# Kernel optimization log

Hardware: AMD Instinct MI355X
Metric: run time of the kernel (lower is better)

## Reference

```python
import jax, jax.numpy as jnp
import numpy as np

B, L, ENC_IN, C_OUT = 4, 2048, 64, 64
D_MODEL, N_HEADS, D_FF, E_LAYERS = 1024, 16, 4096, 4
CA_K = 5  # ChannelAttention1D kernel: int(|log2(1024)+1|/2)=5 (odd)


def _layer_norm(x, w, b, eps=1e-5):
    m = x.mean(-1, keepdims=True)
    v = ((x - m) ** 2).mean(-1, keepdims=True)
    return (x - m) * jax.lax.rsqrt(v + eps) * w + b


def _flow_attention(q, k, v):
    # q,k,v: [B, L, H, D] -> work in [B, H, L, D]
    q = jax.nn.sigmoid(jnp.swapaxes(q, 1, 2))
    k = jax.nn.sigmoid(jnp.swapaxes(k, 1, 2))
    v = jnp.swapaxes(v, 1, 2)
    eps = 1e-6
    Lq = q.shape[2]
    S = k.shape[2]
    nr = 1.0 / jnp.einsum('bhld,bhd->bhl', q + eps, k.sum(axis=2) + eps)
    nc = 1.0 / jnp.einsum('bhsd,bhd->bhs', k + eps, q.sum(axis=2) + eps)
    nrr = jnp.einsum('bhld,bhd->bhl', q + eps, (k * nc[..., None]).sum(axis=2) + eps)
    ncr = jnp.einsum('bhsd,bhd->bhs', k + eps, (q * nr[..., None]).sum(axis=2) + eps)
    nrr = jax.nn.sigmoid(nrr * (float(Lq) / float(S)))
    ncr = jax.nn.softmax(ncr, axis=-1) * S
    kv = jnp.einsum('bhsd,bhse->bhde', k, v * ncr[..., None])  # [B,H,D,Dv]
    out = jnp.einsum('bhld,bhde->bhle', q, kv) * nr[..., None] * nrr[..., None]
    return jnp.swapaxes(out, 1, 2)  # [B, L, H, Dv]


def _token_embed(x, w):
    # x: [B, L, Cin]; circular conv1d kernel=3, pad=1, no bias
    xt = jnp.swapaxes(x, 1, 2)  # [B, Cin, L]
    xt = jnp.concatenate([xt[..., -1:], xt, xt[..., :1]], axis=-1)
    y = jax.lax.conv_general_dilated(xt, w, (1,), 'VALID',
                                     dimension_numbers=('NCH', 'OIH', 'NCH'))
    return jnp.swapaxes(y, 1, 2)  # [B, L, d_model]


def _channel_att(x, w):
    # x: [B, L, C]; squeeze over L, conv over channel axis, sigmoid gate
    y = x.mean(axis=1, keepdims=True)  # [B, 1, C]
    pad = CA_K // 2
    yp = jnp.pad(y, ((0, 0), (0, 0), (pad, pad)))
    yc = jax.lax.conv_general_dilated(yp, w.reshape(1, 1, CA_K), (1,), 'VALID',
                                      dimension_numbers=('NCH', 'OIH', 'NCH'))
    return x * jax.nn.sigmoid(yc)


def _encoder_layer(x, Wq, bq, Wk, bk, Wv, bv, Wo, bo,
                   ln1w, ln1b, ln2w, ln2b, c1w, c1b, c2w, c2b):
    Bx, Lx, _ = x.shape
    q = (x @ Wq.T + bq).reshape(Bx, Lx, N_HEADS, -1)
    k = (x @ Wk.T + bk).reshape(Bx, Lx, N_HEADS, -1)
    v = (x @ Wv.T + bv).reshape(Bx, Lx, N_HEADS, -1)
    a = _flow_attention(q, k, v).reshape(Bx, Lx, -1)
    a = a @ Wo.T + bo
    x = _layer_norm(x + a, ln1w, ln1b)
    y = jax.nn.relu(jnp.einsum('bld,fd->blf', x, c1w) + c1b)  # conv1 k=1
    y = jnp.einsum('blf,df->bld', y, c2w) + c2b               # conv2 k=1
    return _layer_norm(x + y, ln2w, ln2b)


def setup_inputs() -> dict:
    key = jax.random.key(0)
    ks = jax.random.split(key, 16)
    s = 0.02
    E, D, F = E_LAYERS, D_MODEL, D_FF
    inp = {
        'x': jax.random.normal(ks[0], (B, L, ENC_IN), jnp.float32),
        'tok_conv_w': jax.random.normal(ks[1], (D, ENC_IN, 3), jnp.float32) * s,
        'Wq': jax.random.normal(ks[2], (E, D, D), jnp.float32) * s,
        'bq': jnp.zeros((E, D), jnp.float32),
        'Wk': jax.random.normal(ks[3], (E, D, D), jnp.float32) * s,
        'bk': jnp.zeros((E, D), jnp.float32),
        'Wv': jax.random.normal(ks[4], (E, D, D), jnp.float32) * s,
        'bv': jnp.zeros((E, D), jnp.float32),
        'Wo': jax.random.normal(ks[5], (E, D, D), jnp.float32) * s,
        'bo': jnp.zeros((E, D), jnp.float32),
        'conv1_w': jax.random.normal(ks[6], (E, F, D), jnp.float32) * s,
        'conv1_b': jnp.zeros((E, F), jnp.float32),
        'conv2_w': jax.random.normal(ks[7], (E, D, F), jnp.float32) * s,
        'conv2_b': jnp.zeros((E, D), jnp.float32),
        'ln1_w': jnp.ones((E, D), jnp.float32),
        'ln1_b': jnp.zeros((E, D), jnp.float32),
        'ln2_w': jnp.ones((E, D), jnp.float32),
        'ln2_b': jnp.zeros((E, D), jnp.float32),
        'ca_w': jax.random.normal(ks[8], (E, CA_K), jnp.float32) * 0.2,
        'lnf_w': jnp.ones((D,), jnp.float32),
        'lnf_b': jnp.zeros((D,), jnp.float32),
        'proj_w': jax.random.normal(ks[9], (C_OUT, D), jnp.float32) * s,
        'proj_b': jnp.zeros((C_OUT,), jnp.float32),
    }
    return inp


def reference(x, tok_conv_w, Wq, bq, Wk, bk, Wv, bv, Wo, bo,
              conv1_w, conv1_b, conv2_w, conv2_b,
              ln1_w, ln1_b, ln2_w, ln2_b, ca_w,
              lnf_w, lnf_b, proj_w, proj_b):
    h = _token_embed(x, tok_conv_w)  # dropout = identity (eval)
    for i in range(E_LAYERS):
        h = _encoder_layer(h, Wq[i], bq[i], Wk[i], bk[i], Wv[i], bv[i], Wo[i], bo[i],
                           ln1_w[i], ln1_b[i], ln2_w[i], ln2_b[i],
                           conv1_w[i], conv1_b[i], conv2_w[i], conv2_b[i])
        h = _channel_att(h, ca_w[i])
    # Encoder re-applies the last attention layer after the conv loop (faithful)
    i = E_LAYERS - 1
    h = _encoder_layer(h, Wq[i], bq[i], Wk[i], bk[i], Wv[i], bv[i], Wo[i], bo[i],
                       ln1_w[i], ln1_b[i], ln2_w[i], ln2_b[i],
                       conv1_w[i], conv1_b[i], conv2_w[i], conv2_b[i])
    h = _layer_norm(h, lnf_w, lnf_b)
    return h @ proj_w.T + proj_b
```

## Files before the change

kernel.cpp:

```cpp
#include <hip/hip_runtime.h>
#include <stdint.h>

#define L_SEQ 2048
#define DM 1024
#define NH 16
#define DFF 4096
#define NB 4
#define ROWS (NB * L_SEQ)

typedef __attribute__((ext_vector_type(8))) __bf16 bf16x8;
typedef __attribute__((ext_vector_type(4))) float f32x4;

__device__ __forceinline__ float bf2f(unsigned short u) {
  union { unsigned int i; float f; } x; x.i = ((unsigned int)u) << 16; return x.f;
}
__device__ __forceinline__ unsigned short f2bf(float f) {
  union { float f; unsigned int i; } x; x.f = f;
  unsigned int r = x.i + 0x7FFFu + ((x.i >> 16) & 1u);
  return (unsigned short)(r >> 16);
}

typedef __attribute__((address_space(3))) void lds_void;
typedef const __attribute__((address_space(1))) void gbl_void;

__device__ __forceinline__ void stage16(const void* g, void* ldsbase) {
  __builtin_amdgcn_global_load_lds((gbl_void*)g, (lds_void*)ldsbase, 16, 0, 0);
}

__global__ __launch_bounds__(256)
void gemm_bt(const unsigned short* __restrict__ A,
             const unsigned short* __restrict__ B,
             const float* __restrict__ bias,
             unsigned short* __restrict__ C16,
             float* __restrict__ C32,
             int K, int lda, int ldc, int n_limit, int act)
{
  __shared__ __attribute__((aligned(16))) unsigned short As[128 * 32];
  __shared__ __attribute__((aligned(16))) unsigned short Bs[128 * 32];
  const int tid  = threadIdx.x;
  const int wave = tid >> 6, lane = tid & 63;
  const int wm = (wave & 1) << 6, wn = (wave >> 1) << 6;
  const int l16 = lane & 15, quad = lane >> 4;

  const unsigned short* Ab = A + (size_t)blockIdx.x * 128 * lda;
  const unsigned short* Bb = B + (size_t)blockIdx.y * 128 * K;

  const int srow = (wave << 4) + (lane >> 2);
  const int scol = (lane & 3) << 3;

  f32x4 acc[4][4] = {};

  for (int k0 = 0; k0 < K; k0 += 32) {
    const size_t aoff = (size_t)srow * lda + k0 + scol;
    const size_t boff = (size_t)srow * K   + k0 + scol;
    stage16(Ab + aoff,                    &As[(wave * 16) * 32]);
    stage16(Ab + aoff + (size_t)64 * lda, &As[(wave * 16 + 64) * 32]);
    stage16(Bb + boff,                    &Bs[(wave * 16) * 32]);
    stage16(Bb + boff + (size_t)64 * K,   &Bs[(wave * 16 + 64) * 32]);
    __syncthreads();

    bf16x8 af[4], bfr[4];
#pragma unroll
    for (int mi = 0; mi < 4; mi++)
      af[mi] = *(const bf16x8*)&As[(wm + mi * 16 + l16) * 32 + quad * 8];
#pragma unroll
    for (int ni = 0; ni < 4; ni++)
      bfr[ni] = *(const bf16x8*)&Bs[(wn + ni * 16 + l16) * 32 + quad * 8];
#pragma unroll
    for (int mi = 0; mi < 4; mi++)
#pragma unroll
      for (int ni = 0; ni < 4; ni++)
        acc[mi][ni] = __builtin_amdgcn_mfma_f32_16x16x32_bf16(af[mi], bfr[ni], acc[mi][ni], 0, 0, 0);
    __syncthreads();
  }

  const int row0 = (int)blockIdx.x * 128 + wm + quad * 4;
  const int col0 = (int)blockIdx.y * 128 + wn + l16;
#pragma unroll
  for (int ni = 0; ni < 4; ni++) {
    const int col = col0 + ni * 16;
    if (col >= n_limit) continue;
    const float bv = bias ? bias[col] : 0.0f;
    const bool sig = (act == 2) || (act == 3 && col < 2048);
#pragma unroll
    for (int mi = 0; mi < 4; mi++) {
#pragma unroll
      for (int r = 0; r < 4; r++) {
        const int row = row0 + mi * 16 + r;
        float v = acc[mi][ni][r] + bv;
        if (act == 1) v = fmaxf(v, 0.0f);
        else if (sig) v = 1.0f / (1.0f + __expf(-v));
        if (C32) C32[(size_t)row * ldc + col] = v;
        if (C16) C16[(size_t)row * ldc + col] = f2bf(v);
      }
    }
  }
}

#define AFRAG(bb, mi, ks) (*(const bf16x8*)(smb + (bb) + ((mi) << 11) + ((ks) << 10) + lb))
#define BFRAG(bb, nj, ks) (*(const bf16x8*)(smb + (bb) + 32768 + ((nj) << 11) + ((ks) << 10) + lb))

#define LOAD_A(bb, qm) \
  fa[0][0] = AFRAG(bb, wm8 + (qm)*4 + 0, 0); fa[0][1] = AFRAG(bb, wm8 + (qm)*4 + 0, 1); \
  fa[1][0] = AFRAG(bb, wm8 + (qm)*4 + 1, 0); fa[1][1] = AFRAG(bb, wm8 + (qm)*4 + 1, 1); \
  fa[2][0] = AFRAG(bb, wm8 + (qm)*4 + 2, 0); fa[2][1] = AFRAG(bb, wm8 + (qm)*4 + 2, 1); \
  fa[3][0] = AFRAG(bb, wm8 + (qm)*4 + 3, 0); fa[3][1] = AFRAG(bb, wm8 + (qm)*4 + 3, 1);

#define LOAD_B(bb, qn) \
  fb[(qn)*2+0][0] = BFRAG(bb, wn4 + (qn)*2 + 0, 0); fb[(qn)*2+0][1] = BFRAG(bb, wn4 + (qn)*2 + 0, 1); \
  fb[(qn)*2+1][0] = BFRAG(bb, wn4 + (qn)*2 + 1, 0); fb[(qn)*2+1][1] = BFRAG(bb, wn4 + (qn)*2 + 1, 1);

#define MM(mi, nj) \
  acc[mi][nj] = __builtin_amdgcn_mfma_f32_16x16x32_bf16(fa[(mi)&3][0], fb[nj][0], acc[mi][nj], 0, 0, 0); \
  acc[mi][nj] = __builtin_amdgcn_mfma_f32_16x16x32_bf16(fa[(mi)&3][1], fb[nj][1], acc[mi][nj], 0, 0, 0);

#define MFMA_QUAD(qm, qn) \
  MM((qm)*4+0, (qn)*2+0) MM((qm)*4+0, (qn)*2+1) \
  MM((qm)*4+1, (qn)*2+0) MM((qm)*4+1, (qn)*2+1) \
  MM((qm)*4+2, (qn)*2+0) MM((qm)*4+2, (qn)*2+1) \
  MM((qm)*4+3, (qn)*2+0) MM((qm)*4+3, (qn)*2+1)

#define PH_MFMA(qm, qn) \
  __builtin_amdgcn_s_barrier(); \
  asm volatile("s_waitcnt lgkmcnt(0)" ::: "memory"); \
  __builtin_amdgcn_sched_barrier(0); \
  __builtin_amdgcn_s_setprio(1); \
  MFMA_QUAD(qm, qn); \
  __builtin_amdgcn_s_setprio(0); \
  __builtin_amdgcn_sched_barrier(0); \
  __builtin_amdgcn_s_barrier();

__global__ __launch_bounds__(512, 2)
void gemm256(const unsigned short* __restrict__ A,
             const unsigned short* __restrict__ B,
             const float* __restrict__ bias,
             unsigned short* __restrict__ C16,
             float* __restrict__ C32,
             int K, int lda, int ldc, int n_limit, int act, int nb)
{
  __shared__ __attribute__((aligned(16))) unsigned short sm[65536];
  char* smb = (char*)sm;

  const int tid  = threadIdx.x;
  const int wave = tid >> 6, lane = tid & 63;
  const int l16 = lane & 15, quad = lane >> 4;
  const int lb = lane << 4;
  const int wm = wave >> 2, wn = wave & 3;
  const int wm8 = wm * 8, wn4 = wn * 4;

  const int nwg  = (int)gridDim.x;
  const int orig = (int)blockIdx.x;
  const int qq = nwg >> 3, rr = nwg & 7;
  const int xcd = orig & 7, loc = orig >> 3;
  const int wgid = (xcd < rr ? xcd * (qq + 1) : rr * (qq + 1) + (xcd - rr) * qq) + loc;
  const int bx = wgid / nb, by = wgid % nb;

  const unsigned short* Ab = A + (size_t)bx * 256 * lda;
  const unsigned short* Bb = B + (size_t)by * 256 * K;

  const int rb0 = ((wave >> 1) << 4) + l16;
  const int cb0 = ((wave & 1) << 5) + (quad << 3);

  const int T = K >> 6;

  auto stageHalf = [&](int bufbyte, int h, int t) {
    const unsigned short* src;
    size_t ld;
    if (h < 2) { ld = (size_t)lda; src = Ab + (size_t)((h & 1) * 128 + rb0) * ld + (size_t)t * 64 + cb0; }
    else       { ld = (size_t)K;   src = Bb + (size_t)((h & 1) * 128 + rb0) * ld + (size_t)t * 64 + cb0; }
    char* dst = smb + bufbyte + h * 16384 + wave * 1024;
    stage16(src, dst);
    stage16(src + 64 * ld, dst + 8192);
  };

  bf16x8 fa[4][2], fb[4][2];
  f32x4 acc[8][4] = {};

  stageHalf(0, 0, 0); stageHalf(0, 1, 0); stageHalf(0, 2, 0); stageHalf(0, 3, 0);
  if (T > 1) {
    stageHalf(1 << 16, 0, 1);
    asm volatile("s_waitcnt vmcnt(2)" ::: "memory");
  } else {
    asm volatile("s_waitcnt vmcnt(0)" ::: "memory");
  }
  __builtin_amdgcn_sched_barrier(0);
  __builtin_amdgcn_s_barrier();

  for (int t = 0; t < T; ++t) {
    const int bb  = (t & 1) << 16;
    const int nbb = bb ^ (1 << 16);
    const bool st1 = (t + 1 < T), st2 = (t + 2 < T);

    LOAD_A(bb, 0)
    LOAD_B(bb, 0)
    if (st1) stageHalf(nbb, 1, t + 1);
    PH_MFMA(0, 0)

    LOAD_B(bb, 1)
    if (st1) stageHalf(nbb, 2, t + 1);
    PH_MFMA(0, 1)

    LOAD_A(bb, 1)
    if (st1) stageHalf(nbb, 3, t + 1);
    PH_MFMA(1, 1)

    if (st2) {
      stageHalf(bb, 0, t + 2);
      asm volatile("s_waitcnt vmcnt(2)" ::: "memory");
    } else {
      asm volatile("s_waitcnt vmcnt(0)" ::: "memory");
    }
    __builtin_amdgcn_sched_barrier(0);
    __builtin_amdgcn_s_barrier();
    __builtin_amdgcn_s_setprio(1);
    MFMA_QUAD(1, 0)
    __builtin_amdgcn_s_setprio(0);
    __builtin_amdgcn_sched_barrier(0);
    __builtin_amdgcn_s_barrier();
  }

  const int row0 = bx * 256 + wm * 128 + quad * 4;
  const int col0 = by * 256 + wn * 64 + l16;
#pragma unroll
  for (int nj = 0; nj < 4; ++nj) {
    const int col = col0 + nj * 16;
    if (col >= n_limit) continue;
    const float bv = bias ? bias[col] : 0.0f;
    const bool sig = (act == 2) || (act == 3 && col < 2048);
#pragma unroll
    for (int mi = 0; mi < 8; ++mi) {
#pragma unroll
      for (int r = 0; r < 4; ++r) {
        const int row = row0 + mi * 16 + r;
        float v = acc[mi][nj][r] + bv;
        if (act == 1) v = fmaxf(v, 0.0f);
        else if (sig) v = 1.0f / (1.0f + __expf(-v));
        if (C32) C32[(size_t)row * ldc + col] = v;
        if (C16) C16[(size_t)row * ldc + col] = f2bf(v);
      }
    }
  }
}


__global__ __launch_bounds__(256)
void fa_sums(const unsigned short* __restrict__ Q, const unsigned short* __restrict__ K,
             int ld, float* __restrict__ ksp, float* __restrict__ qsp)
{
  const int bh = blockIdx.x, chunk = blockIdx.y;
  const size_t base = ((size_t)(bh >> 4) * L_SEQ) * ld + (size_t)(bh & 15) * 64;
  const int t = threadIdx.x, lane = t & 63, wave = t >> 6;
  __shared__ float red[256];
  float ks = 0.f, qs = 0.f;
  const int l0 = chunk * 256 + wave * 64;
  for (int i = 0; i < 64; i++) {
    const size_t idx = base + (size_t)(l0 + i) * ld + lane;
    ks += bf2f(K[idx]);
    qs += bf2f(Q[idx]);
  }
  red[t] = ks; __syncthreads();
  if (t < 64) ksp[(bh * 8 + chunk) * 64 + t] = red[t] + red[t + 64] + red[t + 128] + red[t + 192];
  __syncthreads();
  red[t] = qs; __syncthreads();
  if (t < 64) qsp[(bh * 8 + chunk) * 64 + t] = red[t] + red[t + 64] + red[t + 128] + red[t + 192];
}

__global__ __launch_bounds__(256)
void fa_rows1(const unsigned short* __restrict__ Q, const unsigned short* __restrict__ K,
              int ld, const float* __restrict__ ksp, const float* __restrict__ qsp,
              float* __restrict__ nr, float* __restrict__ t1p, float* __restrict__ t2p)
{
  const int bh = blockIdx.x, chunk = blockIdx.y;
  const size_t base = ((size_t)(bh >> 4) * L_SEQ) * ld + (size_t)(bh & 15) * 64;
  const int t = threadIdx.x, lane = t & 63, wave = t >> 6;
  const float eps = 1e-6f;
  __shared__ float s_kse[64], s_qse[64], red[256];
  if (t < 64) {
    float s = 0.f;
    for (int j = 0; j < 8; j++) s += ksp[(bh * 8 + j) * 64 + t];
    s_kse[t] = s + eps;
  } else if (t < 128) {
    const int d = t - 64;
    float s = 0.f;
    for (int j = 0; j < 8; j++) s += qsp[(bh * 8 + j) * 64 + d];
    s_qse[d] = s + eps;
  }
  __syncthreads();
  const float kse = s_kse[lane], qse = s_qse[lane];
  float t1a = 0.f, t2a = 0.f;
  for (int i = 0; i < 32; i++) {
    const int l = chunk * 128 + wave + 4 * i;
    const size_t idx = base + (size_t)l * ld + lane;
    const float q = bf2f(Q[idx]), k = bf2f(K[idx]);
    float a = (q + eps) * kse;
    float c = (k + eps) * qse;
#pragma unroll
    for (int off = 32; off; off >>= 1) { a += __shfl_xor(a, off); c += __shfl_xor(c, off); }
    const float nrl = 1.f / a, ncl = 1.f / c;
    if (lane == 0) nr[bh * L_SEQ + l] = nrl;
    t1a += k * ncl;
    t2a += q * nrl;
  }
  red[t] = t1a; __syncthreads();
  if (t < 64) t1p[(bh * 16 + chunk) * 64 + t] = red[t] + red[t + 64] + red[t + 128] + red[t + 192];
  __syncthreads();
  red[t] = t2a; __syncthreads();
  if (t < 64) t2p[(bh * 16 + chunk) * 64 + t] = red[t] + red[t + 64] + red[t + 128] + red[t + 192];
}

__global__ __launch_bounds__(256)
void fa_rows2(const unsigned short* __restrict__ Q, const unsigned short* __restrict__ K,
              int ld, const float* __restrict__ t1p, const float* __restrict__ t2p,
              float* __restrict__ nr, float* __restrict__ sc)
{
  const int bh = blockIdx.x, chunk = blockIdx.y;
  const size_t base = ((size_t)(bh >> 4) * L_SEQ) * ld + (size_t)(bh & 15) * 64;
  const int t = threadIdx.x, lane = t & 63, wave = t >> 6;
  const float eps = 1e-6f;
  __shared__ float s_t1e[64], s_t2e[64];
  if (t < 64) {
    float s = 0.f;
    for (int j = 0; j < 16; j++) s += t1p[(bh * 16 + j) * 64 + t];
    s_t1e[t] = s + eps;
  } else if (t < 128) {
    const int d = t - 64;
    float s = 0.f;
    for (int j = 0; j < 16; j++) s += t2p[(bh * 16 + j) * 64 + d];
    s_t2e[d] = s + eps;
  }
  __syncthreads();
  const float t1e = s_t1e[lane], t2e = s_t2e[lane];
  for (int i = 0; i < 32; i++) {
    const int l = chunk * 128 + wave + 4 * i;
    const size_t idx = base + (size_t)l * ld + lane;
    const float q = bf2f(Q[idx]), k = bf2f(K[idx]);
    float a = (q + eps) * t1e;
    float c = (k + eps) * t2e;
#pragma unroll
    for (int off = 32; off; off >>= 1) { a += __shfl_xor(a, off); c += __shfl_xor(c, off); }
    if (lane == 0) {
      nr[bh * L_SEQ + l] *= 1.f / (1.f + __expf(-a));
      sc[bh * L_SEQ + l] = c;
    }
  }
}

__global__ __launch_bounds__(256)
void fa_softmax(float* __restrict__ sc, float* __restrict__ kv)
{
  const int bh = blockIdx.x, t = threadIdx.x;
  __shared__ float red[256];
  float4* kvz = (float4*)(kv + bh * 64 * 64);
  for (int j = 0; j < 4; j++) kvz[t + 256 * j] = make_float4(0.f, 0.f, 0.f, 0.f);

  float* row = sc + bh * L_SEQ;
  float m = -3.4e38f;
  for (int l = t; l < L_SEQ; l += 256) m = fmaxf(m, row[l]);
  red[t] = m; __syncthreads();
  for (int s = 128; s > 0; s >>= 1) { if (t < s) red[t] = fmaxf(red[t], red[t + s]); __syncthreads(); }
  const float mx = red[0];
  __syncthreads();
  float ps = 0.f;
  float pv[8];
#pragma unroll
  for (int j = 0; j < 8; j++) {
    const int l = t + 256 * j;
    pv[j] = __expf(row[l] - mx);
    ps += pv[j];
  }
  red[t] = ps; __syncthreads();
  for (int s = 128; s > 0; s >>= 1) { if (t < s) red[t] += red[t + s]; __syncthreads(); }
  const float scale = (float)L_SEQ / red[0];
#pragma unroll
  for (int j = 0; j < 8; j++) row[t + 256 * j] = pv[j] * scale;
}

__global__ __launch_bounds__(256)
void fa_kv(const unsigned short* __restrict__ K, const unsigned short* __restrict__ V,
           int ld, const float* __restrict__ sc, float* __restrict__ kv)
{
  const int bh = blockIdx.x, chunk = blockIdx.y;
  const size_t base = ((size_t)(bh >> 4) * L_SEQ) * ld + (size_t)(bh & 15) * 64;
  const int t = threadIdx.x, lane = t & 63, wave = t >> 6;
  const int l16 = lane & 15, quad = lane >> 4;
  __shared__ __attribute__((aligned(16))) unsigned short s_kT[64 * 72];
  __shared__ __attribute__((aligned(16))) unsigned short s_vT[64 * 72];

  f32x4 acc5[4] = {};
  for (int sub = 0; sub < 2; sub++) {
    const int l0 = chunk * 128 + sub * 64;
#pragma unroll
    for (int it = 0; it < 4; it++) {
      const int task = it * 256 + t;
      const int l = task >> 4;
      const int g = task & 15;
      const size_t gidx = base + (size_t)(l0 + l) * ld + g * 4;
      const ushort4 k4 = *(const ushort4*)(K + gidx);
      const ushort4 v4 = *(const ushort4*)(V + gidx);
      const float wgt = sc[bh * L_SEQ + l0 + l];
      s_kT[(g * 4 + 0) * 72 + l] = k4.x;
      s_kT[(g * 4 + 1) * 72 + l] = k4.y;
      s_kT[(g * 4 + 2) * 72 + l] = k4.z;
      s_kT[(g * 4 + 3) * 72 + l] = k4.w;
      s_vT[(g * 4 + 0) * 72 + l] = f2bf(bf2f(v4.x) * wgt);
      s_vT[(g * 4 + 1) * 72 + l] = f2bf(bf2f(v4.y) * wgt);
      s_vT[(g * 4 + 2) * 72 + l] = f2bf(bf2f(v4.z) * wgt);
      s_vT[(g * 4 + 3) * 72 + l] = f2bf(bf2f(v4.w) * wgt);
    }
    __syncthreads();
#pragma unroll
    for (int ks = 0; ks < 2; ks++) {
      const bf16x8 af = *(const bf16x8*)&s_kT[(wave * 16 + l16) * 72 + ks * 32 + quad * 8];
#pragma unroll
      for (int et = 0; et < 4; et++) {
        const bf16x8 bf = *(const bf16x8*)&s_vT[(et * 16 + l16) * 72 + ks * 32 + quad * 8];
        acc5[et] = __builtin_amdgcn_mfma_f32_16x16x32_bf16(af, bf, acc5[et], 0, 0, 0);
      }
    }
    __syncthreads();
  }
#pragma unroll
  for (int et = 0; et < 4; et++)
#pragma unroll
    for (int r = 0; r < 4; r++)
      atomicAdd(&kv[bh * 4096 + (wave * 16 + quad * 4 + r) * 64 + et * 16 + l16], acc5[et][r]);
}

__global__ __launch_bounds__(256)
void fa_out(const unsigned short* __restrict__ Q, int ld, const float* __restrict__ kv,
            const float* __restrict__ nr, unsigned short* O)
{
  const int bh = blockIdx.x, chunk = blockIdx.y;
  const size_t base = ((size_t)(bh >> 4) * L_SEQ) * ld + (size_t)(bh & 15) * 64;
  const int t = threadIdx.x, lane = t & 63, wave = t >> 6;
  const int l16 = lane & 15, quad = lane >> 4;
  __shared__ __attribute__((aligned(16))) unsigned short s_kvT[64 * 72];

#pragma unroll
  for (int j = 0; j < 16; j++) {
    const int i = t + 256 * j;
    const int d = i >> 6, e = i & 63;
    s_kvT[e * 72 + d] = f2bf(kv[bh * 4096 + i]);
  }
  __syncthreads();

  bf16x8 bfr6[4][2];
#pragma unroll
  for (int et = 0; et < 4; et++)
#pragma unroll
    for (int ks = 0; ks < 2; ks++)
      bfr6[et][ks] = *(const bf16x8*)&s_kvT[(et * 16 + l16) * 72 + ks * 32 + quad * 8];

#pragma unroll
  for (int ti = 0; ti < 2; ti++) {
    const int l0 = chunk * 128 + (wave * 2 + ti) * 16;
    f32x4 oc[4] = {};
#pragma unroll
    for (int ks = 0; ks < 2; ks++) {
      const bf16x8 aq = *(const bf16x8*)(Q + base + (size_t)(l0 + l16) * ld + ks * 32 + quad * 8);
#pragma unroll
      for (int et = 0; et < 4; et++)
        oc[et] = __builtin_amdgcn_mfma_f32_16x16x32_bf16(aq, bfr6[et][ks], oc[et], 0, 0, 0);
    }
#pragma unroll
    for (int r = 0; r < 4; r++) {
      const int l = l0 + quad * 4 + r;
      const float scl = nr[bh * L_SEQ + l];
#pragma unroll
      for (int et = 0; et < 4; et++)
        O[base + (size_t)l * ld + et * 16 + l16] = f2bf(oc[et][r] * scl);
    }
  }
}

__global__ __launch_bounds__(256)
void ln_fused(const float* res, const float* __restrict__ add,
              const float* __restrict__ w, const float* __restrict__ bb,
              float* out32, unsigned short* out16)
{
  const int row = blockIdx.x * 4 + (threadIdx.x >> 6);
  const int lane = threadIdx.x & 63;
  const size_t roff = (size_t)row * DM;
  const float4* rp = (const float4*)(res + roff);
  const float4* ap = add ? (const float4*)(add + roff) : nullptr;

  float x[16], s = 0.f, s2 = 0.f;
#pragma unroll
  for (int q4 = 0; q4 < 4; q4++) {
    float4 v = rp[lane * 4 + q4];
    if (ap) { float4 a = ap[lane * 4 + q4]; v.x += a.x; v.y += a.y; v.z += a.z; v.w += a.w; }
    x[q4 * 4 + 0] = v.x; x[q4 * 4 + 1] = v.y; x[q4 * 4 + 2] = v.z; x[q4 * 4 + 3] = v.w;
    s += v.x + v.y + v.z + v.w;
    s2 += v.x * v.x + v.y * v.y + v.z * v.z + v.w * v.w;
  }
#pragma unroll
  for (int off = 32; off; off >>= 1) { s += __shfl_xor(s, off); s2 += __shfl_xor(s2, off); }
  const float mean = s * (1.f / DM);
  const float var = s2 * (1.f / DM) - mean * mean;
  const float rstd = rsqrtf(var + 1e-5f);
#pragma unroll
  for (int j = 0; j < 16; j++) {
    const int c = lane * 16 + j;
    x[j] = (x[j] - mean) * rstd * w[c] + bb[c];
  }
  if (out32) {
    float4* op = (float4*)(out32 + roff);
#pragma unroll
    for (int q4 = 0; q4 < 4; q4++) {
      float4 v; v.x = x[q4*4+0]; v.y = x[q4*4+1]; v.z = x[q4*4+2]; v.w = x[q4*4+3];
      op[lane * 4 + q4] = v;
    }
  }
  if (out16) {
#pragma unroll
    for (int q4 = 0; q4 < 4; q4++) {
      ushort4 u;
      u.x = f2bf(x[q4*4+0]); u.y = f2bf(x[q4*4+1]); u.z = f2bf(x[q4*4+2]); u.w = f2bf(x[q4*4+3]);
      *(ushort4*)(out16 + roff + lane * 16 + q4 * 4) = u;
    }
  }
}

__global__ void ca_zero(float* __restrict__ ybar) {
  const int i = blockIdx.x * 256 + threadIdx.x;
  if (i < NB * DM) ybar[i] = 0.f;
}
__global__ void ca_mean(const unsigned short* __restrict__ H16, float* __restrict__ ybar) {
  const int b = blockIdx.x, cc = blockIdx.y, lc = blockIdx.z;
  const int c = cc * 256 + threadIdx.x;
  float s = 0.f;
  for (int l = lc * 256; l < lc * 256 + 256; l++)
    s += bf2f(H16[((size_t)(b * L_SEQ + l)) * DM + c]);
  atomicAdd(&ybar[b * DM + c], s);
}
__global__ void ca_gate(const float* __restrict__ ybar, const float* __restrict__ cw,
                        float* __restrict__ gate) {
  const int i = blockIdx.x * 256 + threadIdx.x;
  if (i >= NB * DM) return;
  const int b = i >> 10, c = i & 1023;
  float acc = 0.f;
#pragma unroll
  for (int j = 0; j < 5; j++) {
    const int cc = c + j - 2;
    const float yv = (cc >= 0 && cc < DM) ? ybar[b * DM + cc] * (1.f / L_SEQ) : 0.f;
    acc += cw[j] * yv;
  }
  gate[i] = 1.f / (1.f + __expf(-acc));
}
__global__ void ca_apply(float* __restrict__ H32, unsigned short* __restrict__ H16,
                         const float* __restrict__ gate) {
  const size_t i = ((size_t)blockIdx.x * 256 + threadIdx.x) * 4;
  const int row = (int)(i >> 10);
  const int b = row >> 11;
  const int c = (int)(i & 1023);
  float4 v = *(float4*)(H32 + i);
  v.x *= gate[b * DM + c + 0];
  v.y *= gate[b * DM + c + 1];
  v.z *= gate[b * DM + c + 2];
  v.w *= gate[b * DM + c + 3];
  *(float4*)(H32 + i) = v;
  unsigned short* hp = H16 + i;
  hp[0] = f2bf(v.x); hp[1] = f2bf(v.y); hp[2] = f2bf(v.z); hp[3] = f2bf(v.w);
}

__global__ void embed_gather(const float* __restrict__ x, unsigned short* __restrict__ Ae) {
  const int i = blockIdx.x * 256 + threadIdx.x;
  if (i >= ROWS * 192) return;
  const int row = i / 192, kk = i % 192;
  const int t3 = kk >> 6, c = kk & 63;
  const int b = row >> 11, l = row & 2047;
  const int ls = (l + t3 - 1 + L_SEQ) & 2047;
  Ae[i] = f2bf(x[((size_t)(b * L_SEQ + ls)) * 64 + c]);
}
__global__ void embed_repack(const float* __restrict__ w, unsigned short* __restrict__ We) {
  const int i = blockIdx.x * 256 + threadIdx.x;
  if (i >= DM * 192) return;
  const int f = i / 192, kk = i % 192;
  const int t3 = kk >> 6, c = kk & 63;
  We[i] = f2bf(w[(f * 64 + c) * 3 + t3]);
}
__global__ void pad_proj(const float* __restrict__ pw, unsigned short* __restrict__ Wp) {
  const int i = blockIdx.x * 256 + threadIdx.x;
  if (i >= 128 * DM) return;
  Wp[i] = ((i >> 10) < 64) ? f2bf(pw[i]) : (unsigned short)0;
}
__global__ void pack_qkv_bias(const float* __restrict__ bq, const float* __restrict__ bk,
                              const float* __restrict__ bv, float* __restrict__ bqkv) {
  const int i = blockIdx.x * 256 + threadIdx.x;
  if (i >= 3072) return;
  bqkv[i] = (i < 1024) ? bq[i] : (i < 2048 ? bk[i - 1024] : bv[i - 2048]);
}
__global__ void cvt_layer_weights(const float* __restrict__ Wq, const float* __restrict__ Wk,
                                  const float* __restrict__ Wv, const float* __restrict__ Wo,
                                  const float* __restrict__ c1, const float* __restrict__ c2,
                                  unsigned short* __restrict__ Wl, unsigned short* __restrict__ WlFF) {
  const int g = blockIdx.x * 256 + threadIdx.x;
  const int i = g << 2;
  const float* src; unsigned short* dst;
  if (i < (1 << 22)) {
    const int w = i >> 20, off = i & ((1 << 20) - 1);
    const float* srcs[4] = {Wq, Wk, Wv, Wo};
    src = srcs[w] + off; dst = Wl + (w << 20) + off;
  } else {
    const int j = i - (1 << 22);
    const int w = j >> 22, off = j & ((1 << 22) - 1);
    src = (w ? c2 : c1) + off; dst = WlFF + (w << 22) + off;
  }
  const float4 v = *(const float4*)src;
  ushort4 u; u.x = f2bf(v.x); u.y = f2bf(v.y); u.z = f2bf(v.z); u.w = f2bf(v.w);
  *(ushort4*)dst = u;
}

extern "C" void kernel_launch(void* const* d_in, const int* in_sizes, int n_in,
                              void* d_out, int out_size, void* d_ws, size_t ws_size,
                              hipStream_t stream) {
  const float* x     = (const float*)d_in[0];
  const float* tokw  = (const float*)d_in[1];
  const float* Wq    = (const float*)d_in[2];
  const float* bq    = (const float*)d_in[3];
  const float* Wk    = (const float*)d_in[4];
  const float* bk    = (const float*)d_in[5];
  const float* Wv    = (const float*)d_in[6];
  const float* bv    = (const float*)d_in[7];
  const float* Wo    = (const float*)d_in[8];
  const float* bo    = (const float*)d_in[9];
  const float* c1w   = (const float*)d_in[10];
  const float* c1b   = (const float*)d_in[11];
  const float* c2w   = (const float*)d_in[12];
  const float* c2b   = (const float*)d_in[13];
  const float* ln1w  = (const float*)d_in[14];
  const float* ln1b  = (const float*)d_in[15];
  const float* ln2w  = (const float*)d_in[16];
  const float* ln2b  = (const float*)d_in[17];
  const float* caw   = (const float*)d_in[18];
  const float* lnfw  = (const float*)d_in[19];
  const float* lnfb  = (const float*)d_in[20];
  const float* projw = (const float*)d_in[21];
  const float* projb = (const float*)d_in[22];

  char* ws = (char*)d_ws;
  float*          R32 = (float*)(ws);
  unsigned short* R16 = (unsigned short*)(ws + ((size_t)32 << 20));
  float*          A32 = (float*)(ws + ((size_t)48 << 20));
  unsigned short* U   = (unsigned short*)(ws + ((size_t)80 << 20));
  unsigned short* QKV16 = U;
  unsigned short* F16   = U;
  char* fa = ws + ((size_t)128 << 20);
  float* fa_nr  = (float*)(fa);
  float* fa_sc  = (float*)(fa + (512 << 10));
  float* fa_ksp = (float*)(fa + (1024 << 10));
  float* fa_qsp = (float*)(fa + (1152 << 10));
  float* fa_t1p = (float*)(fa + (1280 << 10));
  float* fa_t2p = (float*)(fa + (1792 << 10));
  float* fa_kvb = (float*)(fa + (2304 << 10));
  unsigned short* Wl   = (unsigned short*)(ws + ((size_t)144 << 20));
  unsigned short* WlFF = (unsigned short*)(ws + ((size_t)152 << 20));
  char* misc = ws + ((size_t)168 << 20);
  float*          ybar = (float*)misc;
  float*          gate = (float*)(misc + (16 << 10));
  float*          bqkv = (float*)(misc + (32 << 10));
  unsigned short* We   = (unsigned short*)(misc + (64 << 10));
  unsigned short* Wp   = (unsigned short*)(misc + (512 << 10));

  const int BIG = 1 << 30;
  auto gemm = [&](const unsigned short* A, const unsigned short* B, const float* bias,
                  unsigned short* C16, float* C32, int N, int K, int lda, int ldc,
                  int nlim, int act) {
    if ((N & 255) == 0 && (K & 63) == 0) {
      const int nb = N >> 8;
      const int nwg = (ROWS >> 8) * nb;
      gemm256<<<dim3(nwg), dim3(512), 0, stream>>>(A, B, bias, C16, C32, K, lda, ldc, nlim, act, nb);
    } else {
      dim3 grid(ROWS / 128, N / 128);
      gemm_bt<<<grid, dim3(256), 0, stream>>>(A, B, bias, C16, C32, K, lda, ldc, nlim, act);
    }
  };

  embed_gather<<<(ROWS * 192 + 255) / 256, 256, 0, stream>>>(x, U);
  embed_repack<<<(DM * 192 + 255) / 256, 256, 0, stream>>>(tokw, We);
  gemm(U, We, nullptr, R16, R32, DM, 192, 192, DM, BIG, 0);

  for (int it = 0; it < 5; it++) {
    const int i = (it < 4) ? it : 3;
    if (it != 4) {
      cvt_layer_weights<<<(3 << 20) / 256, 256, 0, stream>>>(
          Wq + ((size_t)i << 20), Wk + ((size_t)i << 20),
          Wv + ((size_t)i << 20), Wo + ((size_t)i << 20),
          c1w + ((size_t)i << 22), c2w + ((size_t)i << 22), Wl, WlFF);
      pack_qkv_bias<<<12, 256, 0, stream>>>(bq + i * DM, bk + i * DM, bv + i * DM, bqkv);
    }
    const unsigned short* Wo16 = Wl + (3 << 20);
    const unsigned short* C116 = WlFF;
    const unsigned short* C216 = WlFF + (1 << 22);

    gemm(R16, Wl, bqkv, QKV16, nullptr, 3072, DM, DM, 3072, BIG, 3);

    const unsigned short* Qp = QKV16;
    const unsigned short* Kp = QKV16 + 1024;
    unsigned short*       Vp = QKV16 + 2048;

    fa_sums   <<<dim3(64, 8),  256, 0, stream>>>(Qp, Kp, 3072, fa_ksp, fa_qsp);
    fa_rows1  <<<dim3(64, 16), 256, 0, stream>>>(Qp, Kp, 3072, fa_ksp, fa_qsp, fa_nr, fa_t1p, fa_t2p);
    fa_rows2  <<<dim3(64, 16), 256, 0, stream>>>(Qp, Kp, 3072, fa_t1p, fa_t2p, fa_nr, fa_sc);
    fa_softmax<<<dim3(64),     256, 0, stream>>>(fa_sc, fa_kvb);
    fa_kv     <<<dim3(64, 16), 256, 0, stream>>>(Kp, Vp, 3072, fa_sc, fa_kvb);
    fa_out    <<<dim3(64, 16), 256, 0, stream>>>(Qp, 3072, fa_kvb, fa_nr, Vp);

    gemm(Vp, Wo16, bo + i * DM, nullptr, A32, DM, DM, 3072, DM, BIG, 0);
    ln_fused<<<ROWS / 4, 256, 0, stream>>>(R32, A32, ln1w + i * DM, ln1b + i * DM, R32, R16);
    gemm(R16, C116, c1b + i * DFF, F16, nullptr, DFF, DM, DM, DFF, BIG, 1);
    gemm(F16, C216, c2b + i * DM, nullptr, A32, DM, DFF, DFF, DM, BIG, 0);
    ln_fused<<<ROWS / 4, 256, 0, stream>>>(R32, A32, ln2w + i * DM, ln2b + i * DM, R32, R16);

    if (it < 4) {
      ca_zero<<<16, 256, 0, stream>>>(ybar);
      ca_mean<<<dim3(NB, 4, 8), 256, 0, stream>>>(R16, ybar);
      ca_gate<<<16, 256, 0, stream>>>(ybar, caw + i * 5, gate);
      ca_apply<<<(ROWS * DM / 4) / 256, 256, 0, stream>>>(R32, R16, gate);
    }
  }

  ln_fused<<<ROWS / 4, 256, 0, stream>>>(R32, nullptr, lnfw, lnfb, nullptr, U);
  pad_proj<<<(128 * DM + 255) / 256, 256, 0, stream>>>(projw, Wp);
  gemm(U, Wp, projb, nullptr, (float*)d_out, 128, DM, DM, 64, 64, 0);

  (void)in_sizes; (void)n_in; (void)out_size; (void)ws_size;
}
```

Measured before the change: 3.159 ms.

## Add pipelined 128x128 GEMM for small-N shapes and deepen gemm256 prefetch

Replaces the simple gemm_bt kernel with a new gemm128 kernel. gemm128 uses 64-wide K tiles, double-buffered global_load_lds staging, an XCD-aware workgroup remap and phased MFMA blocks with barriers. The dispatcher now sends N<3072 GEMMs (e.g. N=1024 projections, embed, N=64 proj) to gemm128 instead of gemm256, which gives more workgroups for better CU occupancy. gemm256 now stages the whole next tile upfront and prefetches two tiles ahead with vmcnt(8). Risks: the N=64 output projection and the K=192 embed shapes rely on gemm128 handling the n_limit and K bounds correctly.

```diff
diff --git a/kernel.cpp b/kernel.cpp
--- a/kernel.cpp
+++ b/kernel.cpp
@@ -27,75 +27,7 @@
   __builtin_amdgcn_global_load_lds((gbl_void*)g, (lds_void*)ldsbase, 16, 0, 0);
 }
 
-__global__ __launch_bounds__(256)
-void gemm_bt(const unsigned short* __restrict__ A,
-             const unsigned short* __restrict__ B,
-             const float* __restrict__ bias,
-             unsigned short* __restrict__ C16,
-             float* __restrict__ C32,
-             int K, int lda, int ldc, int n_limit, int act)
-{
-  __shared__ __attribute__((aligned(16))) unsigned short As[128 * 32];
-  __shared__ __attribute__((aligned(16))) unsigned short Bs[128 * 32];
-  const int tid  = threadIdx.x;
-  const int wave = tid >> 6, lane = tid & 63;
-  const int wm = (wave & 1) << 6, wn = (wave >> 1) << 6;
-  const int l16 = lane & 15, quad = lane >> 4;
-
-  const unsigned short* Ab = A + (size_t)blockIdx.x * 128 * lda;
-  const unsigned short* Bb = B + (size_t)blockIdx.y * 128 * K;
-
-  const int srow = (wave << 4) + (lane >> 2);
-  const int scol = (lane & 3) << 3;
-
-  f32x4 acc[4][4] = {};
-
-  for (int k0 = 0; k0 < K; k0 += 32) {
-    const size_t aoff = (size_t)srow * lda + k0 + scol;
-    const size_t boff = (size_t)srow * K   + k0 + scol;
-    stage16(Ab + aoff,                    &As[(wave * 16) * 32]);
-    stage16(Ab + aoff + (size_t)64 * lda, &As[(wave * 16 + 64) * 32]);
-    stage16(Bb + boff,                    &Bs[(wave * 16) * 32]);
-    stage16(Bb + boff + (size_t)64 * K,   &Bs[(wave * 16 + 64) * 32]);
-    __syncthreads();
-
-    bf16x8 af[4], bfr[4];
-#pragma unroll
-    for (int mi = 0; mi < 4; mi++)
-      af[mi] = *(const bf16x8*)&As[(wm + mi * 16 + l16) * 32 + quad * 8];
-#pragma unroll
-    for (int ni = 0; ni < 4; ni++)
-      bfr[ni] = *(const bf16x8*)&Bs[(wn + ni * 16 + l16) * 32 + quad * 8];
-#pragma unroll
-    for (int mi = 0; mi < 4; mi++)
-#pragma unroll
-      for (int ni = 0; ni < 4; ni++)
-        acc[mi][ni] = __builtin_amdgcn_mfma_f32_16x16x32_bf16(af[mi], bfr[ni], acc[mi][ni], 0, 0, 0);
-    __syncthreads();
-  }
-
-  const int row0 = (int)blockIdx.x * 128 + wm + quad * 4;
-  const int col0 = (int)blockIdx.y * 128 + wn + l16;
-#pragma unroll
-  for (int ni = 0; ni < 4; ni++) {
-    const int col = col0 + ni * 16;
-    if (col >= n_limit) continue;
-    const float bv = bias ? bias[col] : 0.0f;
-    const bool sig = (act == 2) || (act == 3 && col < 2048);
-#pragma unroll
-    for (int mi = 0; mi < 4; mi++) {
-#pragma unroll
-      for (int r = 0; r < 4; r++) {
-        const int row = row0 + mi * 16 + r;
-        float v = acc[mi][ni][r] + bv;
-        if (act == 1) v = fmaxf(v, 0.0f);
-        else if (sig) v = 1.0f / (1.0f + __expf(-v));
-        if (C32) C32[(size_t)row * ldc + col] = v;
-        if (C16) C16[(size_t)row * ldc + col] = f2bf(v);
-      }
-    }
-  }
-}
+#define MFMA1(d, a, b) (d) = __builtin_amdgcn_mfma_f32_16x16x32_bf16((a), (b), (d), 0, 0, 0)
 
 #define AFRAG(bb, mi, ks) (*(const bf16x8*)(smb + (bb) + ((mi) << 11) + ((ks) << 10) + lb))
 #define BFRAG(bb, nj, ks) (*(const bf16x8*)(smb + (bb) + 32768 + ((nj) << 11) + ((ks) << 10) + lb))
@@ -120,12 +52,13 @@
   MM((qm)*4+2, (qn)*2+0) MM((qm)*4+2, (qn)*2+1) \
   MM((qm)*4+3, (qn)*2+0) MM((qm)*4+3, (qn)*2+1)
 
-#define PH_MFMA(qm, qn) \
+#define PH_OPEN \
   __builtin_amdgcn_s_barrier(); \
   asm volatile("s_waitcnt lgkmcnt(0)" ::: "memory"); \
   __builtin_amdgcn_sched_barrier(0); \
-  __builtin_amdgcn_s_setprio(1); \
-  MFMA_QUAD(qm, qn); \
+  __builtin_amdgcn_s_setprio(1);
+
+#define PH_CLOSE \
   __builtin_amdgcn_s_setprio(0); \
   __builtin_amdgcn_sched_barrier(0); \
   __builtin_amdgcn_s_barrier();
@@ -178,8 +111,9 @@
 
   stageHalf(0, 0, 0); stageHalf(0, 1, 0); stageHalf(0, 2, 0); stageHalf(0, 3, 0);
   if (T > 1) {
-    stageHalf(1 << 16, 0, 1);
-    asm volatile("s_waitcnt vmcnt(2)" ::: "memory");
+    stageHalf(1 << 16, 0, 1); stageHalf(1 << 16, 1, 1);
+    stageHalf(1 << 16, 2, 1); stageHalf(1 << 16, 3, 1);
+    asm volatile("s_waitcnt vmcnt(8)" ::: "memory");
   } else {
     asm volatile("s_waitcnt vmcnt(0)" ::: "memory");
   }
@@ -187,26 +121,29 @@
   __builtin_amdgcn_s_barrier();
 
   for (int t = 0; t < T; ++t) {
-    const int bb  = (t & 1) << 16;
-    const int nbb = bb ^ (1 << 16);
-    const bool st1 = (t + 1 < T), st2 = (t + 2 < T);
+    const int bb = (t & 1) << 16;
+    const bool st2 = (t + 2 < T);
 
     LOAD_A(bb, 0)
     LOAD_B(bb, 0)
-    if (st1) stageHalf(nbb, 1, t + 1);
-    PH_MFMA(0, 0)
+    PH_OPEN
+    MFMA_QUAD(0, 0)
+    PH_CLOSE
 
     LOAD_B(bb, 1)
-    if (st1) stageHalf(nbb, 2, t + 1);
-    PH_MFMA(0, 1)
+    PH_OPEN
+    MFMA_QUAD(0, 1)
+    PH_CLOSE
 
     LOAD_A(bb, 1)
-    if (st1) stageHalf(nbb, 3, t + 1);
-    PH_MFMA(1, 1)
+    if (st2) { stageHalf(bb, 2, t + 2); stageHalf(bb, 3, t + 2); }
+    PH_OPEN
+    MFMA_QUAD(1, 1)
+    PH_CLOSE
 
     if (st2) {
-      stageHalf(bb, 0, t + 2);
-      asm volatile("s_waitcnt vmcnt(2)" ::: "memory");
+      stageHalf(bb, 0, t + 2); stageHalf(bb, 1, t + 2);
+      asm volatile("s_waitcnt vmcnt(8)" ::: "memory");
     } else {
       asm volatile("s_waitcnt vmcnt(0)" ::: "memory");
     }
@@ -214,9 +151,7 @@
     __builtin_amdgcn_s_barrier();
     __builtin_amdgcn_s_setprio(1);
     MFMA_QUAD(1, 0)
-    __builtin_amdgcn_s_setprio(0);
-    __builtin_amdgcn_sched_barrier(0);
-    __builtin_amdgcn_s_barrier();
+    PH_CLOSE
   }
 
   const int row0 = bx * 256 + wm * 128 + quad * 4;
@@ -229,6 +164,152 @@
     const bool sig = (act == 2) || (act == 3 && col < 2048);
 #pragma unroll
     for (int mi = 0; mi < 8; ++mi) {
+#pragma unroll
+      for (int r = 0; r < 4; ++r) {
+        const int row = row0 + mi * 16 + r;
+        float v = acc[mi][nj][r] + bv;
+        if (act == 1) v = fmaxf(v, 0.0f);
+        else if (sig) v = 1.0f / (1.0f + __expf(-v));
+        if (C32) C32[(size_t)row * ldc + col] = v;
+        if (C16) C16[(size_t)row * ldc + col] = f2bf(v);
+      }
+    }
+  }
+}
+
+#define AFRAG1(bb, mig, ks) (*(const bf16x8*)(smb + (bb) + (((mig) * 2 + (ks)) << 10) + lb))
+#define BFRAG1(bb, njg, ks) (*(const bf16x8*)(smb + (bb) + 16384 + (((njg) * 2 + (ks)) << 10) + lb))
+
+#define PH128(...) \
+  __builtin_amdgcn_s_barrier(); \
+  asm volatile("s_waitcnt lgkmcnt(0)" ::: "memory"); \
+  __builtin_amdgcn_sched_barrier(0); \
+  __builtin_amdgcn_s_setprio(1); \
+  __VA_ARGS__ \
+  __builtin_amdgcn_s_setprio(0); \
+  __builtin_amdgcn_sched_barrier(0); \
+  __builtin_amdgcn_s_barrier();
+
+__global__ __launch_bounds__(256, 2)
+void gemm128(const unsigned short* __restrict__ A,
+             const unsigned short* __restrict__ B,
+             const float* __restrict__ bias,
+             unsigned short* __restrict__ C16,
+             float* __restrict__ C32,
+             int K, int lda, int ldc, int n_limit, int act, int nb)
+{
+  __shared__ __attribute__((aligned(16))) unsigned short sm[32768];
+  char* smb = (char*)sm;
+  const int tid  = threadIdx.x;
+  const int wave = tid >> 6, lane = tid & 63;
+  const int l16 = lane & 15, quad = lane >> 4;
+  const int lb = lane << 4;
+  const int wm = wave >> 1, wn = wave & 1;
+  const int wm4 = wm * 4, wn4 = wn * 4;
+
+  const int nwg  = (int)gridDim.x;
+  const int orig = (int)blockIdx.x;
+  const int qq = nwg >> 3, rr = nwg & 7;
+  const int xcd = orig & 7, loc = orig >> 3;
+  const int wgid = (xcd < rr ? xcd * (qq + 1) : rr * (qq + 1) + (xcd - rr) * qq) + loc;
+  const int bx = wgid / nb, by = wgid % nb;
+
+  const unsigned short* Ab = A + (size_t)bx * 128 * lda;
+  const unsigned short* Bb = B + (size_t)by * 128 * K;
+
+  const int rb0 = ((wave >> 1) << 4) + l16;
+  const int cb0 = ((wave & 1) << 5) + (quad << 3);
+
+  const int T = K >> 6;
+
+  auto stageA = [&](int bufbyte, int t) {
+    const unsigned short* s0 = Ab + (size_t)rb0 * lda + (size_t)t * 64 + cb0;
+    char* d = smb + bufbyte + wave * 1024;
+    stage16(s0, d);
+    stage16(s0 + (size_t)32 * lda, d + 4096);
+    stage16(s0 + (size_t)64 * lda, d + 8192);
+    stage16(s0 + (size_t)96 * lda, d + 12288);
+  };
+  auto stageB = [&](int bufbyte, int t) {
+    const unsigned short* s0 = Bb + (size_t)rb0 * K + (size_t)t * 64 + cb0;
+    char* d = smb + bufbyte + 16384 + wave * 1024;
+    stage16(s0, d);
+    stage16(s0 + (size_t)32 * K, d + 4096);
+    stage16(s0 + (size_t)64 * K, d + 8192);
+    stage16(s0 + (size_t)96 * K, d + 12288);
+  };
+
+  bf16x8 fa[2][2], fb01[2][2], fb23[2][2];
+  f32x4 acc[4][4] = {};
+
+  stageA(0, 0); stageB(0, 0);
+  if (T > 1) {
+    stageA(32768, 1); stageB(32768, 1);
+    asm volatile("s_waitcnt vmcnt(8)" ::: "memory");
+  } else {
+    asm volatile("s_waitcnt vmcnt(0)" ::: "memory");
+  }
+  __builtin_amdgcn_sched_barrier(0);
+  __builtin_amdgcn_s_barrier();
+
+  for (int t = 0; t < T; ++t) {
+    const int bb = (t & 1) << 15;
+    const bool st2 = (t + 2 < T);
+
+    fa[0][0] = AFRAG1(bb, wm4 + 0, 0); fa[0][1] = AFRAG1(bb, wm4 + 0, 1);
+    fa[1][0] = AFRAG1(bb, wm4 + 1, 0); fa[1][1] = AFRAG1(bb, wm4 + 1, 1);
+    fb01[0][0] = BFRAG1(bb, wn4 + 0, 0); fb01[0][1] = BFRAG1(bb, wn4 + 0, 1);
+    fb01[1][0] = BFRAG1(bb, wn4 + 1, 0); fb01[1][1] = BFRAG1(bb, wn4 + 1, 1);
+    PH128(
+      MFMA1(acc[0][0], fa[0][0], fb01[0][0]); MFMA1(acc[0][0], fa[0][1], fb01[0][1]);
+      MFMA1(acc[0][1], fa[0][0], fb01[1][0]); MFMA1(acc[0][1], fa[0][1], fb01[1][1]);
+      MFMA1(acc[1][0], fa[1][0], fb01[0][0]); MFMA1(acc[1][0], fa[1][1], fb01[0][1]);
+      MFMA1(acc[1][1], fa[1][0], fb01[1][0]); MFMA1(acc[1][1], fa[1][1], fb01[1][1]);
+    )
+
+    fb23[0][0] = BFRAG1(bb, wn4 + 2, 0); fb23[0][1] = BFRAG1(bb, wn4 + 2, 1);
+    fb23[1][0] = BFRAG1(bb, wn4 + 3, 0); fb23[1][1] = BFRAG1(bb, wn4 + 3, 1);
+    PH128(
+      MFMA1(acc[0][2], fa[0][0], fb23[0][0]); MFMA1(acc[0][2], fa[0][1], fb23[0][1]);
+      MFMA1(acc[0][3], fa[0][0], fb23[1][0]); MFMA1(acc[0][3], fa[0][1], fb23[1][1]);
+      MFMA1(acc[1][2], fa[1][0], fb23[0][0]); MFMA1(acc[1][2], fa[1][1], fb23[0][1]);
+      MFMA1(acc[1][3], fa[1][0], fb23[1][0]); MFMA1(acc[1][3], fa[1][1], fb23[1][1]);
+    )
+
+    fa[0][0] = AFRAG1(bb, wm4 + 2, 0); fa[0][1] = AFRAG1(bb, wm4 + 2, 1);
+    fa[1][0] = AFRAG1(bb, wm4 + 3, 0); fa[1][1] = AFRAG1(bb, wm4 + 3, 1);
+    if (st2) stageB(bb, t + 2);
+    PH128(
+      MFMA1(acc[2][2], fa[0][0], fb23[0][0]); MFMA1(acc[2][2], fa[0][1], fb23[0][1]);
+      MFMA1(acc[2][3], fa[0][0], fb23[1][0]); MFMA1(acc[2][3], fa[0][1], fb23[1][1]);
+      MFMA1(acc[3][2], fa[1][0], fb23[0][0]); MFMA1(acc[3][2], fa[1][1], fb23[0][1]);
+      MFMA1(acc[3][3], fa[1][0], fb23[1][0]); MFMA1(acc[3][3], fa[1][1], fb23[1][1]);
+    )
+
+    if (st2) {
+      stageA(bb, t + 2);
+      asm volatile("s_waitcnt vmcnt(8)" ::: "memory");
+    } else {
+      asm volatile("s_waitcnt vmcnt(0)" ::: "memory");
+    }
+    PH128(
+      MFMA1(acc[2][0], fa[0][0], fb01[0][0]); MFMA1(acc[2][0], fa[0][1], fb01[0][1]);
+      MFMA1(acc[2][1], fa[0][0], fb01[1][0]); MFMA1(acc[2][1], fa[0][1], fb01[1][1]);
+      MFMA1(acc[3][0], fa[1][0], fb01[0][0]); MFMA1(acc[3][0], fa[1][1], fb01[0][1]);
+      MFMA1(acc[3][1], fa[1][0], fb01[1][0]); MFMA1(acc[3][1], fa[1][1], fb01[1][1]);
+    )
+  }
+
+  const int row0 = bx * 128 + wm * 64 + quad * 4;
+  const int col0 = by * 128 + wn * 64 + l16;
+#pragma unroll
+  for (int nj = 0; nj < 4; ++nj) {
+    const int col = col0 + nj * 16;
+    if (col >= n_limit) continue;
+    const float bv = bias ? bias[col] : 0.0f;
+    const bool sig = (act == 2) || (act == 3 && col < 2048);
+#pragma unroll
+    for (int mi = 0; mi < 4; ++mi) {
 #pragma unroll
       for (int r = 0; r < 4; ++r) {
         const int row = row0 + mi * 16 + r;
@@ -666,13 +747,14 @@
   auto gemm = [&](const unsigned short* A, const unsigned short* B, const float* bias,
                   unsigned short* C16, float* C32, int N, int K, int lda, int ldc,
                   int nlim, int act) {
-    if ((N & 255) == 0 && (K & 63) == 0) {
+    if (N >= 3072) {
       const int nb = N >> 8;
-      const int nwg = (ROWS >> 8) * nb;
-      gemm256<<<dim3(nwg), dim3(512), 0, stream>>>(A, B, bias, C16, C32, K, lda, ldc, nlim, act, nb);
+      gemm256<<<dim3((ROWS >> 8) * nb), dim3(512), 0, stream>>>(
+          A, B, bias, C16, C32, K, lda, ldc, nlim, act, nb);
     } else {
-      dim3 grid(ROWS / 128, N / 128);
-      gemm_bt<<<grid, dim3(256), 0, stream>>>(A, B, bias, C16, C32, K, lda, ldc, nlim, act);
+      const int nb = N >> 7;
+      gemm128<<<dim3((ROWS >> 7) * nb), dim3(256), 0, stream>>>(
+          A, B, bias, C16, C32, K, lda, ldc, nlim, act, nb);
     }
   };
 
```

New measurement: 3.009 ms. -4.8%, faster.
